# Performance work log

Hardware: AMD Instinct MI355X
Metric: run time of the kernel (lower is better)

## Reference

```python
import jax, jax.numpy as jnp
import numpy as np

BINS = 64

def _soft_histogram(x, bins=BINS):
    # x: (B, C, H, W), values expected in [0, 1]
    B, C, H, W = x.shape
    x_flat = x.reshape(B, C, H * W)                       # (B, C, N)
    bin_width = 1.0 / bins
    centers = jnp.linspace(bin_width / 2, 1 - bin_width / 2, bins,
                           dtype=x.dtype)                 # (bins,)
    sigma = bin_width
    # weights: (B, C, N, bins) gaussian kernel around each bin center
    diff = x_flat[..., None] - centers                    # (B, C, N, bins)
    weights = jnp.exp(-(diff ** 2) / (2.0 * sigma ** 2))
    hist = weights.sum(axis=2)                            # (B, C, bins)
    hist = hist / (hist.sum(axis=-1, keepdims=True) + 1e-08)
    return hist


def setup_inputs() -> dict:
    key = jax.random.key(0)
    k1, k2 = jax.random.split(key)
    pred = jax.random.uniform(k1, (4, 3, 512, 512), dtype=jnp.float32)
    target = jax.random.uniform(k2, (4, 3, 512, 512), dtype=jnp.float32)
    return {"pred": pred, "target": target}


def reference(pred, target):
    pred_hist = _soft_histogram(pred)
    target_hist = _soft_histogram(target)
    pred_cdf = jnp.cumsum(pred_hist, axis=-1)
    target_cdf = jnp.cumsum(target_hist, axis=-1)
    return jnp.mean(jnp.abs(pred_cdf - target_cdf))
```

## Files before the change

kernel.cpp:

```cpp
#include <hip/hip_runtime.h>
#include <stdint.h>

#define BINS    64
#define SBINS   256
#define CSTR    65
#define THREADS 128
#define CHUNKS  32
#define NPIX    (512*512)
#define PPB     (NPIX / CHUNKS)
#define ITERS   (PPB / 4 / THREADS)
#define NCH     12
#define NIMG    (2 * NCH)

__global__ __launch_bounds__(THREADS) void hist_kernel(
    const float* __restrict__ pred, const float* __restrict__ target,
    uint32_t* __restrict__ part )
{
    __shared__ uint32_t lh[THREADS * CSTR];
    __shared__ uint32_t red[2 * THREADS];
    const int tid = threadIdx.x;

    uint32_t* col = &lh[tid * CSTR];
    #pragma unroll
    for (int i = 0; i < CSTR; ++i) col[i] = 0u;
    __syncthreads();

    const int chunk = blockIdx.x;
    const int ch    = blockIdx.y;
    const int z     = blockIdx.z;
    const float* src = (z == 0 ? pred : target)
                     + (size_t)ch * NPIX + (size_t)chunk * PPB;
    const float4* src4 = (const float4*)src;

    float4 v = src4[tid];
    #pragma unroll
    for (int k = 0; k < ITERS; ++k) {
        float4 vn = (k + 1 < ITERS) ? src4[(size_t)(k + 1) * THREADS + tid]
                                    : make_float4(0.f, 0.f, 0.f, 0.f);
        float xv[4] = {v.x, v.y, v.z, v.w};
        #pragma unroll
        for (int e = 0; e < 4; ++e) {
            uint32_t kq = (uint32_t)(int)(xv[e] * 256.0f);
            col[kq >> 2] += 1u << ((kq & 3u) << 3);
        }
        v = vn;
    }
    __syncthreads();

    const int d = tid & 63;
    const int g = tid >> 6;
    uint32_t lo = 0u, hi = 0u;
    #pragma unroll 8
    for (int c = 0; c < 64; ++c) {
        uint32_t x = lh[(g * 64 + c) * CSTR + d];
        lo += x & 0x00FF00FFu;
        hi += (x >> 8) & 0x00FF00FFu;
    }
    red[tid] = lo;
    red[THREADS + tid] = hi;
    __syncthreads();

    if (tid < 64) {
        uint32_t tlo = red[tid] + red[tid + 64];
        uint32_t thi = red[THREADS + tid] + red[THREADS + tid + 64];
        uint4 o;
        o.x = tlo & 0xFFFFu;
        o.y = thi & 0xFFFFu;
        o.z = tlo >> 16;
        o.w = thi >> 16;
        uint4* pp = (uint4*)(part + (((size_t)z * NCH + ch) * CHUNKS + chunk) * SBINS);
        pp[tid] = o;
    }
}

__global__ __launch_bounds__(SBINS) void reduce_conv_kernel(
    const uint32_t* __restrict__ part, float* __restrict__ chist )
{
    __shared__ float cnt[SBINS];
    const int ci = blockIdx.x;
    const int s  = threadIdx.x;
    uint32_t tot = 0u;
    #pragma unroll 8
    for (int i = 0; i < CHUNKS; ++i)
        tot += part[((size_t)ci * CHUNKS + i) * SBINS + s];
    cnt[s] = (float)tot;
    __syncthreads();

    if (s < BINS) {
        float h = 0.0f;
        #pragma unroll
        for (int u = -16; u <= 19; ++u) {
            int idx = 4 * s + u;
            if (idx >= 0 && idx < SBINS) {
                float t = (u - 1.5f) * 0.25f;
                h += __expf(-0.5f * t * t) * cnt[idx];
            }
        }
        chist[ci * BINS + s] = h;
    }
}

__global__ __launch_bounds__(256) void finalize_kernel(
    const float* __restrict__ chist, float* __restrict__ out)
{
    __shared__ float wsum[4];
    const int tid  = threadIdx.x;
    const int lane = tid & 63;
    const int w    = tid >> 6;
    float acc = 0.0f;
    for (int c = w * 3; c < w * 3 + 3; ++c) {
        float cp = chist[c * BINS + lane];
        float ct = chist[(NCH + c) * BINS + lane];
        #pragma unroll
        for (int off = 1; off < 64; off <<= 1) {
            float a = __shfl_up(cp, off, 64);
            float b = __shfl_up(ct, off, 64);
            if (lane >= off) { cp += a; ct += b; }
        }
        float sp = __shfl(cp, 63, 64);
        float st = __shfl(ct, 63, 64);
        float diff = fabsf(cp / (sp + 1e-8f) - ct / (st + 1e-8f));
        #pragma unroll
        for (int off = 32; off; off >>= 1)
            diff += __shfl_xor(diff, off, 64);
        acc += diff;
    }
    if (lane == 0) wsum[w] = acc;
    __syncthreads();
    if (tid == 0)
        out[0] = (wsum[0] + wsum[1] + wsum[2] + wsum[3]) / (float)(NCH * BINS);
}

extern "C" void kernel_launch(void* const* d_in, const int* in_sizes, int n_in,
                              void* d_out, int out_size, void* d_ws, size_t ws_size,
                              hipStream_t stream)
{
    const float* pred   = (const float*)d_in[0];
    const float* target = (const float*)d_in[1];
    uint32_t* part  = (uint32_t*)d_ws;
    float*    chist = (float*)(part + (size_t)NIMG * CHUNKS * SBINS);

    hist_kernel<<<dim3(CHUNKS, NCH, 2), THREADS, 0, stream>>>(pred, target, part);
    reduce_conv_kernel<<<NIMG, SBINS, 0, stream>>>(part, chist);
    finalize_kernel<<<1, 256, 0, stream>>>(chist, (float*)d_out);
}
```

Baseline: 18.52 us.

## Fuse reduce and finalize via cooperative launch; batch histogram LDS updates

Merges the per-image reduce/convolution kernel with the single-block finalize kernel into one cooperative kernel. Each block handles one channel's pred/target pair, computes the CDF difference, and uses a grid sync before block 0 sums the partials, saving one kernel launch. The histogram inner loop now issues four LDS reads up front, resolves same-word collisions in registers, and sends duplicate writes to a dummy slot 64. The row stride becomes 66 so each row can be zeroed with 64-bit stores. The risks are the overhead of a cooperative launch and grid sync, plus the extra compare and select work per pixel.

```diff
diff --git a/kernel.cpp b/kernel.cpp
--- a/kernel.cpp
+++ b/kernel.cpp
@@ -1,9 +1,12 @@
 #include <hip/hip_runtime.h>
+#include <hip/hip_cooperative_groups.h>
 #include <stdint.h>
+
+namespace cg = cooperative_groups;
 
 #define BINS    64
 #define SBINS   256
-#define CSTR    65
+#define CSTR    66
 #define THREADS 128
 #define CHUNKS  32
 #define NPIX    (512*512)
@@ -21,8 +24,9 @@
     const int tid = threadIdx.x;
 
     uint32_t* col = &lh[tid * CSTR];
+    uint2* colv = (uint2*)col;
     #pragma unroll
-    for (int i = 0; i < CSTR; ++i) col[i] = 0u;
+    for (int i = 0; i < CSTR / 2; ++i) colv[i] = make_uint2(0u, 0u);
     __syncthreads();
 
     const int chunk = blockIdx.x;
@@ -37,12 +41,30 @@
     for (int k = 0; k < ITERS; ++k) {
         float4 vn = (k + 1 < ITERS) ? src4[(size_t)(k + 1) * THREADS + tid]
                                     : make_float4(0.f, 0.f, 0.f, 0.f);
-        float xv[4] = {v.x, v.y, v.z, v.w};
-        #pragma unroll
-        for (int e = 0; e < 4; ++e) {
-            uint32_t kq = (uint32_t)(int)(xv[e] * 256.0f);
-            col[kq >> 2] += 1u << ((kq & 3u) << 3);
-        }
+        uint32_t kq0 = (uint32_t)(int)(v.x * 256.0f);
+        uint32_t kq1 = (uint32_t)(int)(v.y * 256.0f);
+        uint32_t kq2 = (uint32_t)(int)(v.z * 256.0f);
+        uint32_t kq3 = (uint32_t)(int)(v.w * 256.0f);
+        uint32_t d0 = kq0 >> 2, d1 = kq1 >> 2, d2 = kq2 >> 2, d3 = kq3 >> 2;
+        uint32_t i0 = 1u << ((kq0 & 3u) << 3);
+        uint32_t i1 = 1u << ((kq1 & 3u) << 3);
+        uint32_t i2 = 1u << ((kq2 & 3u) << 3);
+        uint32_t i3 = 1u << ((kq3 & 3u) << 3);
+        uint32_t a0 = col[d0], a1 = col[d1], a2 = col[d2], a3 = col[d3];
+        bool e01 = d0 == d1, e02 = d0 == d2, e03 = d0 == d3;
+        bool e12 = d1 == d2, e13 = d1 == d3, e23 = d2 == d3;
+        uint32_t i1f = i1 + (e01 ? i0 : 0u);
+        uint32_t i2f = i2 + ((!e01 && e02) ? i0 : 0u) + (e12 ? i1f : 0u);
+        uint32_t i3f = i3 + ((!e01 && !e02 && e03) ? i0 : 0u)
+                          + ((!e12 && e13) ? i1f : 0u)
+                          + (e23 ? i2f : 0u);
+        bool s0 = e01 | e02 | e03;
+        bool s1 = e12 | e13;
+        bool s2 = e23;
+        col[s0 ? 64u : d0] = a0 + i0;
+        col[s1 ? 64u : d1] = a1 + i1f;
+        col[s2 ? 64u : d2] = a2 + i2f;
+        col[d3]            = a3 + i3f;
         v = vn;
     }
     __syncthreads();
@@ -73,49 +95,48 @@
     }
 }
 
-__global__ __launch_bounds__(SBINS) void reduce_conv_kernel(
-    const uint32_t* __restrict__ part, float* __restrict__ chist )
+__global__ __launch_bounds__(256) void pairfin_kernel(
+    const uint32_t* __restrict__ part, float* __restrict__ partial,
+    float* __restrict__ out)
 {
-    __shared__ float cnt[SBINS];
+    __shared__ float cntP[SBINS], cntT[SBINS];
+    __shared__ float histP[BINS], histT[BINS];
     const int ci = blockIdx.x;
     const int s  = threadIdx.x;
-    uint32_t tot = 0u;
+
+    uint32_t tp = 0u, tt = 0u;
     #pragma unroll 8
-    for (int i = 0; i < CHUNKS; ++i)
-        tot += part[((size_t)ci * CHUNKS + i) * SBINS + s];
-    cnt[s] = (float)tot;
+    for (int i = 0; i < CHUNKS; ++i) {
+        tp += part[((size_t)ci * CHUNKS + i) * SBINS + s];
+        tt += part[((size_t)(NCH + ci) * CHUNKS + i) * SBINS + s];
+    }
+    cntP[s] = (float)tp;
+    cntT[s] = (float)tt;
     __syncthreads();
 
-    if (s < BINS) {
+    if (s < 2 * BINS) {
+        const int b = s & 63;
+        const float* cnt = (s < BINS) ? cntP : cntT;
         float h = 0.0f;
         #pragma unroll
         for (int u = -16; u <= 19; ++u) {
-            int idx = 4 * s + u;
+            int idx = 4 * b + u;
             if (idx >= 0 && idx < SBINS) {
                 float t = (u - 1.5f) * 0.25f;
                 h += __expf(-0.5f * t * t) * cnt[idx];
             }
         }
-        chist[ci * BINS + s] = h;
+        if (s < BINS) histP[b] = h; else histT[b] = h;
     }
-}
+    __syncthreads();
 
-__global__ __launch_bounds__(256) void finalize_kernel(
-    const float* __restrict__ chist, float* __restrict__ out)
-{
-    __shared__ float wsum[4];
-    const int tid  = threadIdx.x;
-    const int lane = tid & 63;
-    const int w    = tid >> 6;
-    float acc = 0.0f;
-    for (int c = w * 3; c < w * 3 + 3; ++c) {
-        float cp = chist[c * BINS + lane];
-        float ct = chist[(NCH + c) * BINS + lane];
+    if (s < 64) {
+        float cp = histP[s], ct = histT[s];
         #pragma unroll
         for (int off = 1; off < 64; off <<= 1) {
             float a = __shfl_up(cp, off, 64);
             float b = __shfl_up(ct, off, 64);
-            if (lane >= off) { cp += a; ct += b; }
+            if (s >= off) { cp += a; ct += b; }
         }
         float sp = __shfl(cp, 63, 64);
         float st = __shfl(ct, 63, 64);
@@ -123,12 +144,18 @@
         #pragma unroll
         for (int off = 32; off; off >>= 1)
             diff += __shfl_xor(diff, off, 64);
-        acc += diff;
+        if (s == 0) partial[ci] = diff;
     }
-    if (lane == 0) wsum[w] = acc;
-    __syncthreads();
-    if (tid == 0)
-        out[0] = (wsum[0] + wsum[1] + wsum[2] + wsum[3]) / (float)(NCH * BINS);
+
+    cg::this_grid().sync();
+
+    if (blockIdx.x == 0 && s < 64) {
+        float v = (s < NCH) ? partial[s] : 0.0f;
+        #pragma unroll
+        for (int off = 32; off; off >>= 1)
+            v += __shfl_xor(v, off, 64);
+        if (s == 0) out[0] = v / (float)(NCH * BINS);
+    }
 }
 
 extern "C" void kernel_launch(void* const* d_in, const int* in_sizes, int n_in,
@@ -137,10 +164,13 @@
 {
     const float* pred   = (const float*)d_in[0];
     const float* target = (const float*)d_in[1];
-    uint32_t* part  = (uint32_t*)d_ws;
-    float*    chist = (float*)(part + (size_t)NIMG * CHUNKS * SBINS);
+    uint32_t* part    = (uint32_t*)d_ws;
+    float*    partial = (float*)(part + (size_t)NIMG * CHUNKS * SBINS);
+    float*    outp    = (float*)d_out;
 
     hist_kernel<<<dim3(CHUNKS, NCH, 2), THREADS, 0, stream>>>(pred, target, part);
-    reduce_conv_kernel<<<NIMG, SBINS, 0, stream>>>(part, chist);
-    finalize_kernel<<<1, 256, 0, stream>>>(chist, (float*)d_out);
+
+    void* args[] = { (void*)&part, (void*)&partial, (void*)&outp };
+    hipLaunchCooperativeKernel((const void*)pairfin_kernel,
+                               dim3(NCH), dim3(256), args, 0, stream);
 }
```

New measurement: 38.52 us. +108.0%, slower.
